# Kernel tuning notes

Hardware: AMD Instinct MI355X
Metric: run time of the kernel (lower is better)

Reference implementation:

```python
import jax, jax.numpy as jnp
import numpy as np


def _up(x, h, w):
    # bicubic (Keys a=-0.5, matching PIL BICUBIC) resize of [B,H,W] -> [B,h,w]
    return jax.image.resize(x, (x.shape[0], h, w), method='cubic')


def setup_inputs() -> dict:
    key = jax.random.key(0)
    ks = jax.random.split(key, 10)
    B = 64
    inp = {
        'cam_256': jax.random.uniform(ks[0], (B, 256, 256), dtype=jnp.float32),
        'cam_128': jax.random.uniform(ks[1], (B, 128, 128), dtype=jnp.float32),
        'cam_64':  jax.random.uniform(ks[2], (B, 64, 64), dtype=jnp.float32),
        'cam_32':  jax.random.uniform(ks[3], (B, 32, 32), dtype=jnp.float32),
        'w1': jax.random.normal(ks[4], (2,), dtype=jnp.float32),
        'b1': jax.random.normal(ks[5], (1,), dtype=jnp.float32),
        'w2': jax.random.normal(ks[6], (2,), dtype=jnp.float32),
        'b2': jax.random.normal(ks[7], (1,), dtype=jnp.float32),
        'w3': jax.random.normal(ks[8], (2,), dtype=jnp.float32),
        'b3': jax.random.normal(ks[9], (1,), dtype=jnp.float32),
    }
    return inp


def reference(cam_256, cam_128, cam_64, cam_32, w1, b1, w2, b2, w3, b3):
    B = cam_32.shape[0]
    # stage 1: up(32->64), concat with cam_64, 1x1 conv(2->1) + ReLU
    up32 = _up(cam_32, 64, 64)                              # [B,64,64]
    h64 = jax.nn.relu(w1[0] * up32 + w1[1] * cam_64 + b1[0])
    # stage 2: up(64->128), concat with cam_128, 1x1 conv + ReLU
    up64 = _up(h64, 128, 128)
    h128 = jax.nn.relu(w2[0] * up64 + w2[1] * cam_128 + b2[0])
    # stage 3: up(128->256), concat with cam_256, 1x1 conv + ReLU
    up128 = _up(h128, 256, 256)
    h256 = jax.nn.relu(w3[0] * up128 + w3[1] * cam_256 + b3[0])
    # final: bicubic up to 1024; original loop prepends each new image,
    # reversing batch order -> replicate with flip
    out = _up(h256, 1024, 1024)                             # [B,1024,1024]
    out = jnp.flip(out, axis=0)[:, None]                    # [B,1,1024,1024]
    return out
```

## Files before the change

kernel.cpp:

```cpp
#include <hip/hip_runtime.h>

typedef float vfloat4 __attribute__((ext_vector_type(4)));

__device__ __forceinline__ int iclamp(int v, int lo, int hi) {
  return v < lo ? lo : (v > hi ? hi : v);
}

__device__ __forceinline__ void taps4w(int i, int n, float inv, float w[4]) {
  float s = ((float)i + 0.5f) * inv - 0.5f;
  int k0 = (int)floorf(s);
  float sum = 0.f;
#pragma unroll
  for (int t = 0; t < 4; ++t) {
    int j = k0 - 1 + t;
    float d = fabsf(s - (float)j);
    float wt = (d <= 1.f) ? (((1.5f * d - 2.5f) * d) * d + 1.f)
                          : (((-0.5f * d + 2.5f) * d - 4.f) * d + 2.f);
    if (j < 0 || j >= n) wt = 0.f;
    w[t] = wt;
    sum += wt;
  }
  float r = 1.f / sum;
#pragma unroll
  for (int t = 0; t < 4; ++t) w[t] *= r;
}

#define W0_0 (-0.0439453125f)
#define W0_1 ( 0.3896484375f)
#define W0_2 ( 0.7275390625f)
#define W0_3 (-0.0732421875f)
#define W1_0 (-0.0068359375f)
#define W1_1 ( 0.0908203125f)
#define W1_2 ( 0.9638671875f)
#define W1_3 (-0.0478515625f)
#define U_0 (-0.0234375f)
#define U_1 ( 0.2265625f)
#define U_2 ( 0.8671875f)
#define U_3 (-0.0703125f)

__device__ __forceinline__ void up2_cell(const float (&f)[5][5], int k, int g, int n,
                                         float (&o)[2][2]) {
  if (g >= 2 && g <= n - 3 && k >= 2 && k <= n - 3) {
    float v0[5], v1[5];
#pragma unroll
    for (int c = 0; c < 5; ++c) {
      v0[c] = U_0 * f[0][c] + U_1 * f[1][c] + U_2 * f[2][c] + U_3 * f[3][c];
      v1[c] = U_3 * f[1][c] + U_2 * f[2][c] + U_1 * f[3][c] + U_0 * f[4][c];
    }
    o[0][0] = U_0 * v0[0] + U_1 * v0[1] + U_2 * v0[2] + U_3 * v0[3];
    o[0][1] = U_3 * v0[1] + U_2 * v0[2] + U_1 * v0[3] + U_0 * v0[4];
    o[1][0] = U_0 * v1[0] + U_1 * v1[1] + U_2 * v1[2] + U_3 * v1[3];
    o[1][1] = U_3 * v1[1] + U_2 * v1[2] + U_1 * v1[3] + U_0 * v1[4];
  } else {
#pragma unroll
    for (int p = 0; p < 2; ++p) {
      float wy[4];
      taps4w(2 * k + p, n, 0.5f, wy);
      float vv[5];
#pragma unroll
      for (int c = 0; c < 5; ++c)
        vv[c] = wy[0] * f[p][c] + wy[1] * f[p + 1][c] + wy[2] * f[p + 2][c] + wy[3] * f[p + 3][c];
#pragma unroll
      for (int q = 0; q < 2; ++q) {
        float wx[4];
        taps4w(2 * g + q, n, 0.5f, wx);
        o[p][q] = wx[0] * vv[q] + wx[1] * vv[q + 1] + wx[2] * vv[q + 2] + wx[3] * vv[q + 3];
      }
    }
  }
}

__device__ __forceinline__ void up4_cell(const float (&f)[5][5], int k, int g, int n,
                                         float (&o)[4][4]) {
  if (g >= 2 && g <= n - 3 && k >= 2 && k <= n - 3) {
    float vy[4][5];
#pragma unroll
    for (int c = 0; c < 5; ++c) {
      vy[0][c] = W0_0 * f[0][c] + W0_1 * f[1][c] + W0_2 * f[2][c] + W0_3 * f[3][c];
      vy[1][c] = W1_0 * f[0][c] + W1_1 * f[1][c] + W1_2 * f[2][c] + W1_3 * f[3][c];
      vy[2][c] = W1_3 * f[1][c] + W1_2 * f[2][c] + W1_1 * f[3][c] + W1_0 * f[4][c];
      vy[3][c] = W0_3 * f[1][c] + W0_2 * f[2][c] + W0_1 * f[3][c] + W0_0 * f[4][c];
    }
#pragma unroll
    for (int p = 0; p < 4; ++p) {
      o[p][0] = W0_0 * vy[p][0] + W0_1 * vy[p][1] + W0_2 * vy[p][2] + W0_3 * vy[p][3];
      o[p][1] = W1_0 * vy[p][0] + W1_1 * vy[p][1] + W1_2 * vy[p][2] + W1_3 * vy[p][3];
      o[p][2] = W1_3 * vy[p][1] + W1_2 * vy[p][2] + W1_1 * vy[p][3] + W1_0 * vy[p][4];
      o[p][3] = W0_3 * vy[p][1] + W0_2 * vy[p][2] + W0_1 * vy[p][3] + W0_0 * vy[p][4];
    }
  } else {
#pragma unroll
    for (int p = 0; p < 4; ++p) {
      float wy[4];
      taps4w(4 * k + p, n, 0.25f, wy);
      int oy = (p < 2) ? 0 : 1;
      float vv[5];
#pragma unroll
      for (int c = 0; c < 5; ++c)
        vv[c] = wy[0] * f[oy][c] + wy[1] * f[oy + 1][c] + wy[2] * f[oy + 2][c] + wy[3] * f[oy + 3][c];
#pragma unroll
      for (int q = 0; q < 4; ++q) {
        float wx[4];
        taps4w(4 * g + q, n, 0.25f, wx);
        int ox = (q < 2) ? 0 : 1;
        o[p][q] = wx[0] * vv[ox] + wx[1] * vv[ox + 1] + wx[2] * vv[ox + 2] + wx[3] * vv[ox + 3];
      }
    }
  }
}

__global__ void __launch_bounds__(512, 4) fused_all(
    const float* __restrict__ cam256, const float* __restrict__ cam128,
    const float* __restrict__ cam64, const float* __restrict__ cam32,
    const float* __restrict__ w1, const float* __restrict__ b1,
    const float* __restrict__ w2, const float* __restrict__ b2,
    const float* __restrict__ w3, const float* __restrict__ b3,
    float* __restrict__ out) {
  __shared__ float s_h64[16 * 64];
  __shared__ float s_h128[24 * 128];
  __shared__ float s_h256[36 * 256];

  const int tid = threadIdx.x;
  const int slab = blockIdx.x;
  const int b = blockIdx.y;
  const int s = slab * 32;

  const int r_lo = s - 2 < 0 ? 0 : s - 2, r_hi = s + 33 > 255 ? 255 : s + 33;
  const int kr0 = r_lo >> 1, kr1 = r_hi >> 1;
  const int h256_row0 = 2 * kr0;
  const int j_lo = kr0 - 2 < 0 ? 0 : kr0 - 2, j_hi = kr1 + 2 > 127 ? 127 : kr1 + 2;
  const int kj0 = j_lo >> 1, kj1 = j_hi >> 1;
  const int h128_row0 = 2 * kj0;
  const int m_lo = kj0 - 2 < 0 ? 0 : kj0 - 2, m_hi = kj1 + 2 > 63 ? 63 : kj1 + 2;
  const int km0 = m_lo >> 1, km1 = m_hi >> 1;
  const int h64_row0 = 2 * km0;

  const float w1_0 = w1[0], w1_1 = w1[1], b1_0 = b1[0];
  const float w2_0 = w2[0], w2_1 = w2[1], b2_0 = b2[0];
  const float w3_0 = w3[0], w3_1 = w3[1], b3_0 = b3[0];

  {
    const float* c32 = cam32 + (size_t)b * 32 * 32;
    const float* c64 = cam64 + (size_t)b * 64 * 64;
    const int nk = km1 - km0 + 1;
    for (int idx = tid; idx < nk * 32; idx += 512) {
      int k = km0 + (idx >> 5), g = idx & 31;
      float f[5][5];
#pragma unroll
      for (int i = 0; i < 5; ++i) {
        int r = iclamp(k - 2 + i, 0, 31);
#pragma unroll
        for (int c = 0; c < 5; ++c) f[i][c] = c32[r * 32 + iclamp(g - 2 + c, 0, 31)];
      }
      float o[2][2];
      up2_cell(f, k, g, 32, o);
#pragma unroll
      for (int p = 0; p < 2; ++p)
#pragma unroll
        for (int q = 0; q < 2; ++q) {
          int row = 2 * k + p, col = 2 * g + q;
          float h = w1_0 * o[p][q] + w1_1 * c64[row * 64 + col] + b1_0;
          s_h64[(row - h64_row0) * 64 + col] = fmaxf(h, 0.f);
        }
    }
  }
  __syncthreads();

  {
    const float* c128 = cam128 + (size_t)b * 128 * 128;
    const int nk = kj1 - kj0 + 1;
    for (int idx = tid; idx < nk * 64; idx += 512) {
      int k = kj0 + (idx >> 6), g = idx & 63;
      float f[5][5];
#pragma unroll
      for (int i = 0; i < 5; ++i) {
        int r = iclamp(k - 2 + i, 0, 63) - h64_row0;
#pragma unroll
        for (int c = 0; c < 5; ++c) f[i][c] = s_h64[r * 64 + iclamp(g - 2 + c, 0, 63)];
      }
      float o[2][2];
      up2_cell(f, k, g, 64, o);
#pragma unroll
      for (int p = 0; p < 2; ++p)
#pragma unroll
        for (int q = 0; q < 2; ++q) {
          int row = 2 * k + p, col = 2 * g + q;
          float h = w2_0 * o[p][q] + w2_1 * c128[row * 128 + col] + b2_0;
          s_h128[(row - h128_row0) * 128 + col] = fmaxf(h, 0.f);
        }
    }
  }
  __syncthreads();

  {
    const float* c256 = cam256 + (size_t)b * 256 * 256;
    const int nk = kr1 - kr0 + 1;
    for (int idx = tid; idx < nk * 128; idx += 512) {
      int k = kr0 + (idx >> 7), g = idx & 127;
      float f[5][5];
#pragma unroll
      for (int i = 0; i < 5; ++i) {
        int r = iclamp(k - 2 + i, 0, 127) - h128_row0;
#pragma unroll
        for (int c = 0; c < 5; ++c) f[i][c] = s_h128[r * 128 + iclamp(g - 2 + c, 0, 127)];
      }
      float o[2][2];
      up2_cell(f, k, g, 128, o);
#pragma unroll
      for (int p = 0; p < 2; ++p)
#pragma unroll
        for (int q = 0; q < 2; ++q) {
          int row = 2 * k + p, col = 2 * g + q;
          float h = w3_0 * o[p][q] + w3_1 * c256[row * 256 + col] + b3_0;
          s_h256[(row - h256_row0) * 256 + col] = fmaxf(h, 0.f);
        }
    }
  }
  __syncthreads();

  {
    float* outimg = out + (size_t)(63 - b) * 1024 * 1024;
    for (int idx = tid; idx < 32 * 256; idx += 512) {
      int k = s + (idx >> 8), g = idx & 255;
      float f[5][5];
#pragma unroll
      for (int i = 0; i < 5; ++i) {
        int r = iclamp(k - 2 + i, 0, 255) - h256_row0;
#pragma unroll
        for (int c = 0; c < 5; ++c) f[i][c] = s_h256[r * 256 + iclamp(g - 2 + c, 0, 255)];
      }
      float o[4][4];
      up4_cell(f, k, g, 256, o);
#pragma unroll
      for (int p = 0; p < 4; ++p) {
        vfloat4 v = {o[p][0], o[p][1], o[p][2], o[p][3]};
        __builtin_nontemporal_store(v, (vfloat4*)(outimg + (size_t)(4 * k + p) * 1024 + 4 * g));
      }
    }
  }
}

extern "C" void kernel_launch(void* const* d_in, const int* in_sizes, int n_in_,
                              void* d_out, int out_size, void* d_ws, size_t ws_size,
                              hipStream_t stream) {
  const float* cam256 = (const float*)d_in[0];
  const float* cam128 = (const float*)d_in[1];
  const float* cam64  = (const float*)d_in[2];
  const float* cam32  = (const float*)d_in[3];
  const float* w1 = (const float*)d_in[4];
  const float* b1 = (const float*)d_in[5];
  const float* w2 = (const float*)d_in[6];
  const float* b2 = (const float*)d_in[7];
  const float* w3 = (const float*)d_in[8];
  const float* b3 = (const float*)d_in[9];
  float* out = (float*)d_out;

  fused_all<<<dim3(8, 64), 512, 0, stream>>>(cam256, cam128, cam64, cam32,
                                             w1, b1, w2, b2, w3, b3, out);
}
```

Before: 332.6 us.

## Halve slab height, use precomputed edge-class taps, vectorize skip loads

Each block now covers 16 output rows of the 256 map instead of 32, and runs 256 threads in a 16x64 grid. The shared-memory halos and the total block count are resized to match. The runtime taps4w weight computation at image borders is replaced by precomputed per-edge-class coefficient tables selected through ecls, which removes floor, divide and normalisation work. Skip-connection loads become float2 reads. The cost is more recomputation of halo rows in the earlier stages, since each slab now carries proportionally more overlap.

```diff
diff --git a/kernel.cpp b/kernel.cpp
--- a/kernel.cpp
+++ b/kernel.cpp
@@ -6,23 +6,8 @@
   return v < lo ? lo : (v > hi ? hi : v);
 }
 
-__device__ __forceinline__ void taps4w(int i, int n, float inv, float w[4]) {
-  float s = ((float)i + 0.5f) * inv - 0.5f;
-  int k0 = (int)floorf(s);
-  float sum = 0.f;
-#pragma unroll
-  for (int t = 0; t < 4; ++t) {
-    int j = k0 - 1 + t;
-    float d = fabsf(s - (float)j);
-    float wt = (d <= 1.f) ? (((1.5f * d - 2.5f) * d) * d + 1.f)
-                          : (((-0.5f * d + 2.5f) * d - 4.f) * d + 2.f);
-    if (j < 0 || j >= n) wt = 0.f;
-    w[t] = wt;
-    sum += wt;
-  }
-  float r = 1.f / sum;
-#pragma unroll
-  for (int t = 0; t < 4; ++t) w[t] *= r;
+__device__ __forceinline__ int ecls(int g, int n) {
+  return g < 2 ? g : (g >= n - 2 ? g - n + 5 : 2);
 }
 
 #define W0_0 (-0.0439453125f)
@@ -33,83 +18,84 @@
 #define W1_1 ( 0.0908203125f)
 #define W1_2 ( 0.9638671875f)
 #define W1_3 (-0.0478515625f)
+#define A0 ( 1.11194030f)
+#define A1 (-0.11194030f)
+#define B0 ( 1.05223881f)
+#define B1 (-0.05223881f)
+#define C0 ( 0.91985089f)
+#define C1 ( 0.08667288f)
+#define C2 (-0.00652377f)
+#define D0 ( 0.67788899f)
+#define D1 ( 0.36305732f)
+#define D2 (-0.04094632f)
+#define E0 ( 0.37324602f)
+#define E1 ( 0.69691301f)
+#define E2 (-0.07015903f)
+#define F0 ( 0.09020368f)
+#define F1 ( 0.95732299f)
+#define F2 (-0.04752667f)
+
 #define U_0 (-0.0234375f)
 #define U_1 ( 0.2265625f)
 #define U_2 ( 0.8671875f)
 #define U_3 (-0.0703125f)
-
-__device__ __forceinline__ void up2_cell(const float (&f)[5][5], int k, int g, int n,
-                                         float (&o)[2][2]) {
-  if (g >= 2 && g <= n - 3 && k >= 2 && k <= n - 3) {
-    float v0[5], v1[5];
-#pragma unroll
-    for (int c = 0; c < 5; ++c) {
-      v0[c] = U_0 * f[0][c] + U_1 * f[1][c] + U_2 * f[2][c] + U_3 * f[3][c];
-      v1[c] = U_3 * f[1][c] + U_2 * f[2][c] + U_1 * f[3][c] + U_0 * f[4][c];
-    }
-    o[0][0] = U_0 * v0[0] + U_1 * v0[1] + U_2 * v0[2] + U_3 * v0[3];
-    o[0][1] = U_3 * v0[1] + U_2 * v0[2] + U_1 * v0[3] + U_0 * v0[4];
-    o[1][0] = U_0 * v1[0] + U_1 * v1[1] + U_2 * v1[2] + U_3 * v1[3];
-    o[1][1] = U_3 * v1[1] + U_2 * v1[2] + U_1 * v1[3] + U_0 * v1[4];
-  } else {
-#pragma unroll
-    for (int p = 0; p < 2; ++p) {
-      float wy[4];
-      taps4w(2 * k + p, n, 0.5f, wy);
-      float vv[5];
-#pragma unroll
-      for (int c = 0; c < 5; ++c)
-        vv[c] = wy[0] * f[p][c] + wy[1] * f[p + 1][c] + wy[2] * f[p + 2][c] + wy[3] * f[p + 3][c];
-#pragma unroll
-      for (int q = 0; q < 2; ++q) {
-        float wx[4];
-        taps4w(2 * g + q, n, 0.5f, wx);
-        o[p][q] = wx[0] * vv[q] + wx[1] * vv[q + 1] + wx[2] * vv[q + 2] + wx[3] * vv[q + 3];
-      }
-    }
-  }
-}
-
-__device__ __forceinline__ void up4_cell(const float (&f)[5][5], int k, int g, int n,
-                                         float (&o)[4][4]) {
-  if (g >= 2 && g <= n - 3 && k >= 2 && k <= n - 3) {
-    float vy[4][5];
-#pragma unroll
-    for (int c = 0; c < 5; ++c) {
-      vy[0][c] = W0_0 * f[0][c] + W0_1 * f[1][c] + W0_2 * f[2][c] + W0_3 * f[3][c];
-      vy[1][c] = W1_0 * f[0][c] + W1_1 * f[1][c] + W1_2 * f[2][c] + W1_3 * f[3][c];
-      vy[2][c] = W1_3 * f[1][c] + W1_2 * f[2][c] + W1_1 * f[3][c] + W1_0 * f[4][c];
-      vy[3][c] = W0_3 * f[1][c] + W0_2 * f[2][c] + W0_1 * f[3][c] + W0_0 * f[4][c];
-    }
-#pragma unroll
-    for (int p = 0; p < 4; ++p) {
-      o[p][0] = W0_0 * vy[p][0] + W0_1 * vy[p][1] + W0_2 * vy[p][2] + W0_3 * vy[p][3];
-      o[p][1] = W1_0 * vy[p][0] + W1_1 * vy[p][1] + W1_2 * vy[p][2] + W1_3 * vy[p][3];
-      o[p][2] = W1_3 * vy[p][1] + W1_2 * vy[p][2] + W1_1 * vy[p][3] + W1_0 * vy[p][4];
-      o[p][3] = W0_3 * vy[p][1] + W0_2 * vy[p][2] + W0_1 * vy[p][3] + W0_0 * vy[p][4];
-    }
-  } else {
-#pragma unroll
-    for (int p = 0; p < 4; ++p) {
-      float wy[4];
-      taps4w(4 * k + p, n, 0.25f, wy);
-      int oy = (p < 2) ? 0 : 1;
-      float vv[5];
-#pragma unroll
-      for (int c = 0; c < 5; ++c)
-        vv[c] = wy[0] * f[oy][c] + wy[1] * f[oy + 1][c] + wy[2] * f[oy + 2][c] + wy[3] * f[oy + 3][c];
-#pragma unroll
-      for (int q = 0; q < 4; ++q) {
-        float wx[4];
-        taps4w(4 * g + q, n, 0.25f, wx);
-        int ox = (q < 2) ? 0 : 1;
-        o[p][q] = wx[0] * vv[ox] + wx[1] * vv[ox + 1] + wx[2] * vv[ox + 2] + wx[3] * vv[ox + 3];
-      }
-    }
-  }
-}
-
-__global__ void __launch_bounds__(512, 4) fused_all(
+#define Z0 ( 1.08823529f)
+#define Z1 (-0.08823529f)
+#define Y0 ( 0.81021898f)
+#define Y1 ( 0.21167883f)
+#define Y2 (-0.02189781f)
+#define X0 ( 0.22137405f)
+#define X1 ( 0.84732824f)
+#define X2 (-0.06870229f)
+
+__device__ __forceinline__ float tap2(int cls, int p, float f0, float f1,
+                                      float f2, float f3, float f4) {
+  float r;
+  if (cls == 2)      r = (p == 0) ? U_0*f0 + U_1*f1 + U_2*f2 + U_3*f3
+                                  : U_3*f1 + U_2*f2 + U_1*f3 + U_0*f4;
+  else if (cls == 0) r = (p == 0) ? Z0*f2 + Z1*f3
+                                  : Y0*f2 + Y1*f3 + Y2*f4;
+  else if (cls == 1) r = (p == 0) ? X0*f1 + X1*f2 + X2*f3
+                                  : U_3*f1 + U_2*f2 + U_1*f3 + U_0*f4;
+  else if (cls == 3) r = (p == 0) ? U_0*f0 + U_1*f1 + U_2*f2 + U_3*f3
+                                  : X2*f1 + X1*f2 + X0*f3;
+  else               r = (p == 0) ? Y2*f0 + Y1*f1 + Y0*f2
+                                  : Z1*f1 + Z0*f2;
+  return r;
+}
+
+__device__ __forceinline__ float tap4(int cls, int p, float f0, float f1,
+                                      float f2, float f3, float f4) {
+  float r;
+  if (cls == 2)
+    r = (p == 0) ? W0_0*f0 + W0_1*f1 + W0_2*f2 + W0_3*f3
+      : (p == 1) ? W1_0*f0 + W1_1*f1 + W1_2*f2 + W1_3*f3
+      : (p == 2) ? W1_3*f1 + W1_2*f2 + W1_1*f3 + W1_0*f4
+                 : W0_3*f1 + W0_2*f2 + W0_1*f3 + W0_0*f4;
+  else if (cls == 0)
+    r = (p == 0) ? A0*f2 + A1*f3
+      : (p == 1) ? B0*f2 + B1*f3
+      : (p == 2) ? C0*f2 + C1*f3 + C2*f4
+                 : D0*f2 + D1*f3 + D2*f4;
+  else if (cls == 1)
+    r = (p == 0) ? E0*f1 + E1*f2 + E2*f3
+      : (p == 1) ? F0*f1 + F1*f2 + F2*f3
+      : (p == 2) ? W1_3*f1 + W1_2*f2 + W1_1*f3 + W1_0*f4
+                 : W0_3*f1 + W0_2*f2 + W0_1*f3 + W0_0*f4;
+  else if (cls == 3)
+    r = (p == 0) ? W0_0*f0 + W0_1*f1 + W0_2*f2 + W0_3*f3
+      : (p == 1) ? W1_0*f0 + W1_1*f1 + W1_2*f2 + W1_3*f3
+      : (p == 2) ? F2*f1 + F1*f2 + F0*f3
+                 : E2*f1 + E1*f2 + E0*f3;
+  else
+    r = (p == 0) ? D2*f0 + D1*f1 + D0*f2
+      : (p == 1) ? C2*f0 + C1*f1 + C0*f2
+      : (p == 2) ? B1*f1 + B0*f2
+                 : A1*f1 + A0*f2;
+  return r;
+}
+
+__global__ void __launch_bounds__(256, 4) fused_all(
     const float* __restrict__ cam256, const float* __restrict__ cam128,
     const float* __restrict__ cam64, const float* __restrict__ cam32,
     const float* __restrict__ w1, const float* __restrict__ b1,
@@ -117,15 +103,15 @@
     const float* __restrict__ w3, const float* __restrict__ b3,
     float* __restrict__ out) {
   __shared__ float s_h64[16 * 64];
-  __shared__ float s_h128[24 * 128];
-  __shared__ float s_h256[36 * 256];
+  __shared__ float s_h128[18 * 128];
+  __shared__ float s_h256[20 * 256];
 
   const int tid = threadIdx.x;
   const int slab = blockIdx.x;
   const int b = blockIdx.y;
-  const int s = slab * 32;
-
-  const int r_lo = s - 2 < 0 ? 0 : s - 2, r_hi = s + 33 > 255 ? 255 : s + 33;
+  const int s0 = slab * 16;
+
+  const int r_lo = s0 - 2 < 0 ? 0 : s0 - 2, r_hi = s0 + 17 > 255 ? 255 : s0 + 17;
   const int kr0 = r_lo >> 1, kr1 = r_hi >> 1;
   const int h256_row0 = 2 * kr0;
   const int j_lo = kr0 - 2 < 0 ? 0 : kr0 - 2, j_hi = kr1 + 2 > 127 ? 127 : kr1 + 2;
@@ -143,8 +129,9 @@
     const float* c32 = cam32 + (size_t)b * 32 * 32;
     const float* c64 = cam64 + (size_t)b * 64 * 64;
     const int nk = km1 - km0 + 1;
-    for (int idx = tid; idx < nk * 32; idx += 512) {
+    for (int idx = tid; idx < nk * 32; idx += 256) {
       int k = km0 + (idx >> 5), g = idx & 31;
+      int kcls = ecls(k, 32), gcls = ecls(g, 32);
       float f[5][5];
 #pragma unroll
       for (int i = 0; i < 5; ++i) {
@@ -152,16 +139,19 @@
 #pragma unroll
         for (int c = 0; c < 5; ++c) f[i][c] = c32[r * 32 + iclamp(g - 2 + c, 0, 31)];
       }
-      float o[2][2];
-      up2_cell(f, k, g, 32, o);
-#pragma unroll
-      for (int p = 0; p < 2; ++p)
-#pragma unroll
-        for (int q = 0; q < 2; ++q) {
-          int row = 2 * k + p, col = 2 * g + q;
-          float h = w1_0 * o[p][q] + w1_1 * c64[row * 64 + col] + b1_0;
-          s_h64[(row - h64_row0) * 64 + col] = fmaxf(h, 0.f);
-        }
+#pragma unroll
+      for (int p = 0; p < 2; ++p) {
+        float v[5];
+#pragma unroll
+        for (int c = 0; c < 5; ++c)
+          v[c] = tap2(kcls, p, f[0][c], f[1][c], f[2][c], f[3][c], f[4][c]);
+        float o0 = tap2(gcls, 0, v[0], v[1], v[2], v[3], v[4]);
+        float o1 = tap2(gcls, 1, v[0], v[1], v[2], v[3], v[4]);
+        int row = 2 * k + p;
+        float2 cm = *(const float2*)(c64 + row * 64 + 2 * g);
+        s_h64[(row - h64_row0) * 64 + 2 * g]     = fmaxf(w1_0 * o0 + w1_1 * cm.x + b1_0, 0.f);
+        s_h64[(row - h64_row0) * 64 + 2 * g + 1] = fmaxf(w1_0 * o1 + w1_1 * cm.y + b1_0, 0.f);
+      }
     }
   }
   __syncthreads();
@@ -169,8 +159,9 @@
   {
     const float* c128 = cam128 + (size_t)b * 128 * 128;
     const int nk = kj1 - kj0 + 1;
-    for (int idx = tid; idx < nk * 64; idx += 512) {
+    for (int idx = tid; idx < nk * 64; idx += 256) {
       int k = kj0 + (idx >> 6), g = idx & 63;
+      int kcls = ecls(k, 64), gcls = ecls(g, 64);
       float f[5][5];
 #pragma unroll
       for (int i = 0; i < 5; ++i) {
@@ -178,16 +169,19 @@
 #pragma unroll
         for (int c = 0; c < 5; ++c) f[i][c] = s_h64[r * 64 + iclamp(g - 2 + c, 0, 63)];
       }
-      float o[2][2];
-      up2_cell(f, k, g, 64, o);
-#pragma unroll
-      for (int p = 0; p < 2; ++p)
-#pragma unroll
-        for (int q = 0; q < 2; ++q) {
-          int row = 2 * k + p, col = 2 * g + q;
-          float h = w2_0 * o[p][q] + w2_1 * c128[row * 128 + col] + b2_0;
-          s_h128[(row - h128_row0) * 128 + col] = fmaxf(h, 0.f);
-        }
+#pragma unroll
+      for (int p = 0; p < 2; ++p) {
+        float v[5];
+#pragma unroll
+        for (int c = 0; c < 5; ++c)
+          v[c] = tap2(kcls, p, f[0][c], f[1][c], f[2][c], f[3][c], f[4][c]);
+        float o0 = tap2(gcls, 0, v[0], v[1], v[2], v[3], v[4]);
+        float o1 = tap2(gcls, 1, v[0], v[1], v[2], v[3], v[4]);
+        int row = 2 * k + p;
+        float2 cm = *(const float2*)(c128 + row * 128 + 2 * g);
+        s_h128[(row - h128_row0) * 128 + 2 * g]     = fmaxf(w2_0 * o0 + w2_1 * cm.x + b2_0, 0.f);
+        s_h128[(row - h128_row0) * 128 + 2 * g + 1] = fmaxf(w2_0 * o1 + w2_1 * cm.y + b2_0, 0.f);
+      }
     }
   }
   __syncthreads();
@@ -195,8 +189,9 @@
   {
     const float* c256 = cam256 + (size_t)b * 256 * 256;
     const int nk = kr1 - kr0 + 1;
-    for (int idx = tid; idx < nk * 128; idx += 512) {
+    for (int idx = tid; idx < nk * 128; idx += 256) {
       int k = kr0 + (idx >> 7), g = idx & 127;
+      int kcls = ecls(k, 128), gcls = ecls(g, 128);
       float f[5][5];
 #pragma unroll
       for (int i = 0; i < 5; ++i) {
@@ -204,37 +199,51 @@
 #pragma unroll
         for (int c = 0; c < 5; ++c) f[i][c] = s_h128[r * 128 + iclamp(g - 2 + c, 0, 127)];
       }
-      float o[2][2];
-      up2_cell(f, k, g, 128, o);
-#pragma unroll
-      for (int p = 0; p < 2; ++p)
-#pragma unroll
-        for (int q = 0; q < 2; ++q) {
-          int row = 2 * k + p, col = 2 * g + q;
-          float h = w3_0 * o[p][q] + w3_1 * c256[row * 256 + col] + b3_0;
-          s_h256[(row - h256_row0) * 256 + col] = fmaxf(h, 0.f);
-        }
+#pragma unroll
+      for (int p = 0; p < 2; ++p) {
+        float v[5];
+#pragma unroll
+        for (int c = 0; c < 5; ++c)
+          v[c] = tap2(kcls, p, f[0][c], f[1][c], f[2][c], f[3][c], f[4][c]);
+        float o0 = tap2(gcls, 0, v[0], v[1], v[2], v[3], v[4]);
+        float o1 = tap2(gcls, 1, v[0], v[1], v[2], v[3], v[4]);
+        int row = 2 * k + p;
+        float2 cm = *(const float2*)(c256 + row * 256 + 2 * g);
+        s_h256[(row - h256_row0) * 256 + 2 * g]     = fmaxf(w3_0 * o0 + w3_1 * cm.x + b3_0, 0.f);
+        s_h256[(row - h256_row0) * 256 + 2 * g + 1] = fmaxf(w3_0 * o1 + w3_1 * cm.y + b3_0, 0.f);
+      }
     }
   }
   __syncthreads();
 
   {
     float* outimg = out + (size_t)(63 - b) * 1024 * 1024;
-    for (int idx = tid; idx < 32 * 256; idx += 512) {
-      int k = s + (idx >> 8), g = idx & 255;
-      float f[5][5];
-#pragma unroll
-      for (int i = 0; i < 5; ++i) {
-        int r = iclamp(k - 2 + i, 0, 255) - h256_row0;
-#pragma unroll
-        for (int c = 0; c < 5; ++c) f[i][c] = s_h256[r * 256 + iclamp(g - 2 + c, 0, 255)];
-      }
-      float o[4][4];
-      up4_cell(f, k, g, 256, o);
+    for (int idx = tid; idx < 16 * 256; idx += 256) {
+      int k = s0 + (idx >> 8), g = idx & 255;
+      int kcls = ecls(k, 256), gcls = ecls(g, 256);
+      int rbase[5], cidx[5];
+#pragma unroll
+      for (int i = 0; i < 5; ++i) rbase[i] = (iclamp(k - 2 + i, 0, 255) - h256_row0) * 256;
+#pragma unroll
+      for (int c = 0; c < 5; ++c) cidx[c] = iclamp(g - 2 + c, 0, 255);
+      float f[5][5];
+#pragma unroll
+      for (int i = 0; i < 5; ++i)
+#pragma unroll
+        for (int c = 0; c < 5; ++c) f[i][c] = s_h256[rbase[i] + cidx[c]];
 #pragma unroll
       for (int p = 0; p < 4; ++p) {
-        vfloat4 v = {o[p][0], o[p][1], o[p][2], o[p][3]};
-        __builtin_nontemporal_store(v, (vfloat4*)(outimg + (size_t)(4 * k + p) * 1024 + 4 * g));
+        float v[5];
+#pragma unroll
+        for (int c = 0; c < 5; ++c)
+          v[c] = tap4(kcls, p, f[0][c], f[1][c], f[2][c], f[3][c], f[4][c]);
+        vfloat4 o;
+        o.x = tap4(gcls, 0, v[0], v[1], v[2], v[3], v[4]);
+        o.y = tap4(gcls, 1, v[0], v[1], v[2], v[3], v[4]);
+        o.z = tap4(gcls, 2, v[0], v[1], v[2], v[3], v[4]);
+        o.w = tap4(gcls, 3, v[0], v[1], v[2], v[3], v[4]);
+        __builtin_nontemporal_store(
+            o, (vfloat4*)(outimg + (size_t)(4 * k + p) * 1024 + 4 * g));
       }
     }
   }
@@ -255,6 +264,6 @@
   const float* b3 = (const float*)d_in[9];
   float* out = (float*)d_out;
 
-  fused_all<<<dim3(8, 64), 512, 0, stream>>>(cam256, cam128, cam64, cam32,
-                                             w1, b1, w2, b2, w3, b3, out);
-}
+  fused_all<<<dim3(16, 64), 256, 0, stream>>>(cam256, cam128, cam64, cam32,
+                                              w1, b1, w2, b2, w3, b3, out);
+}
```

New measurement: 353.3 us. 6.2% more time.
